# Optimization experiments

Measured on AMD Instinct MI355X. Metric: run time of the kernel, lower is better.

Reference implementation:

```python
import jax, jax.numpy as jnp
import numpy as np

B, C, D, T, N_SUBJ = 64, 1024, 1024, 1024, 32


def setup_inputs() -> dict:
    key = jax.random.key(0)
    k1, k2, k3 = jax.random.split(key, 3)
    x = jax.random.normal(k1, (B, C, T), dtype=jnp.float32)
    subjects = jax.random.randint(k2, (B,), 0, N_SUBJ, dtype=jnp.int64)
    # weights: normal_() then scaled by 1/sqrt(in_channels), as in __init__
    weights = jax.random.normal(k3, (N_SUBJ, C, D), dtype=jnp.float32) / np.sqrt(C).astype(np.float32)
    return {"x": x, "subjects": subjects, "weights": weights}


def reference(x, subjects, weights):
    # gather per-sample projection matrices: (B, C, D)
    w = weights[subjects]
    # out[b, d, t] = sum_c x[b, c, t] * w[b, c, d]
    return jnp.einsum('bct,bcd->bdt', x, w)
```

## Files before the change

### kernel.cpp

```cpp
#include <hip/hip_runtime.h>
#include <hip/hip_bf16.h>

typedef __attribute__((ext_vector_type(8))) short bf16x8;
typedef __attribute__((ext_vector_type(4))) float f32x4;
typedef __attribute__((ext_vector_type(4))) unsigned u32x4;

#define CDIM 1024
#define DDIM 1024
#define TDIM 1024
#define BK 32

__device__ __forceinline__ unsigned cvt_pk_bf16(float a, float b) {
    unsigned r;
    asm("v_cvt_pk_bf16_f32 %0, %1, %2" : "=v"(r) : "v"(a), "v"(b));
    return r;
}


#define KSTEP(VCUR, VNXT, K0)                                                   \
  {                                                                             \
    const int ksafe = ((K0) + BK) & (CDIM - 1);   \
    _Pragma("unroll")                                                           \
    for (int j = 0; j < 8; ++j)                                                 \
        VNXT[j] = *(const float4*)(sp + ((size_t)(ksafe + (cg << 3) + j) << 10)); \
    u32x4 hg[4], lg[4];                                                         \
    _Pragma("unroll")                                                           \
    for (int rr = 0; rr < 4; ++rr) {                                            \
      _Pragma("unroll")                                                         \
      for (int p = 0; p < 4; ++p) {                                             \
        const float f0 = VCUR[2 * p][rr];                                       \
        const float f1 = VCUR[2 * p + 1][rr];                                   \
        const unsigned h = cvt_pk_bf16(f0, f1);                                 \
        const float l0 = f0 - __uint_as_float(h << 16);                         \
        const float l1 = f1 - __uint_as_float(h & 0xFFFF0000u);                 \
        hg[rr][p] = h;                                                          \
        lg[rr][p] = cvt_pk_bf16(l0, l1);                                        \
      }                                                                         \
    }                                                                           \
    __syncthreads();                                                            \
    _Pragma("unroll")                                                           \
    for (int rr = 0; rr < 4; ++rr) {                                            \
      const int row = col0 + rr;                                                \
      short* sl = slds + row * 64;                                              \
      const int so = ((cg ^ ((row ^ (row >> 3)) & 7)) << 3);                    \
      *(u32x4*)(sl + so) = hg[rr];                                              \
      *(u32x4*)(sl + (so ^ 32)) = lg[rr];                                       \
    }                                                                           \
    __syncthreads();                                                            \
    bf16x8 ah[4], al[4];                                                        \
    _Pragma("unroll")                                                           \
    for (int m = 0; m < 4; ++m) {                                               \
      const short* wrow = Wt + (wdOff + m * 16 + fr) * 64;                      \
      ah[m] = *(const bf16x8*)(wrow + offHW[m]);                                \
      al[m] = *(const bf16x8*)(wrow + (offHW[m] ^ 32));                         \
    }                                                                           \
    _Pragma("unroll")                                                           \
    for (int np = 0; np < 4; ++np) {                                            \
      const int n0 = 2 * np, n1 = 2 * np + 1;                                   \
      const short* xr0 = Xt + (wtOff + n0 * 16 + fr) * 64;                      \
      const short* xr1 = Xt + (wtOff + n1 * 16 + fr) * 64;                      \
      const bf16x8 bh0 = *(const bf16x8*)(xr0 + offHX[n0]);                     \
      const bf16x8 bl0 = *(const bf16x8*)(xr0 + (offHX[n0] ^ 32));              \
      const bf16x8 bh1 = *(const bf16x8*)(xr1 + offHX[n1]);                     \
      const bf16x8 bl1 = *(const bf16x8*)(xr1 + (offHX[n1] ^ 32));              \
      _Pragma("unroll")                                                         \
      for (int m = 0; m < 4; ++m)                                               \
        acc[m][n0] = __builtin_amdgcn_mfma_f32_16x16x32_bf16(ah[m], bh0, acc[m][n0], 0, 0, 0); \
      _Pragma("unroll")                                                         \
      for (int m = 0; m < 4; ++m)                                               \
        acc[m][n1] = __builtin_amdgcn_mfma_f32_16x16x32_bf16(ah[m], bh1, acc[m][n1], 0, 0, 0); \
      _Pragma("unroll")                                                         \
      for (int m = 0; m < 4; ++m)                                               \
        acc[m][n0] = __builtin_amdgcn_mfma_f32_16x16x32_bf16(ah[m], bl0, acc[m][n0], 0, 0, 0); \
      _Pragma("unroll")                                                         \
      for (int m = 0; m < 4; ++m)                                               \
        acc[m][n1] = __builtin_amdgcn_mfma_f32_16x16x32_bf16(ah[m], bl1, acc[m][n1], 0, 0, 0); \
      _Pragma("unroll")                                                         \
      for (int m = 0; m < 4; ++m)                                               \
        acc[m][n0] = __builtin_amdgcn_mfma_f32_16x16x32_bf16(al[m], bh0, acc[m][n0], 0, 0, 0); \
      _Pragma("unroll")                                                         \
      for (int m = 0; m < 4; ++m)                                               \
        acc[m][n1] = __builtin_amdgcn_mfma_f32_16x16x32_bf16(al[m], bh1, acc[m][n1], 0, 0, 0); \
    }                                                                           \
  }

__global__ __launch_bounds__(512, 1)
void subject_gemm(const float* __restrict__ x, const int* __restrict__ subj,
                  const float* __restrict__ w, float* __restrict__ out)
{
    __shared__ short Wt[256 * 64];
    __shared__ short Xt[256 * 64];

    const int bid = blockIdx.x;
    const int xcd = bid & 7;
    const int slot = bid >> 3;
    const int b = (xcd << 3) | (slot >> 4);
    const int r = slot & 15;
    const int dtile = (r >> 2) << 8;
    const int ttile = (r & 3) << 8;

    const int s = subj[b];
    const float* __restrict__ wB = w + (size_t)s * (CDIM * DDIM);
    const float* __restrict__ xB = x + (size_t)b * (CDIM * TDIM);

    const int tid = threadIdx.x;
    const int lane = tid & 63;
    const int wave = tid >> 6;

    const int ht = tid & 255;
    const int tq = ht & 63;
    const int cg = ht >> 6;
    const int col0 = tq << 2;
    const bool isW = (tid < 256);
    const float* sp = (isW ? wB + dtile : xB + ttile) + col0;
    short* slds = (isW ? Wt : Xt);

    const int wdOff = (wave >> 1) << 6;
    const int wtOff = (wave & 1) << 7;
    const int fr = lane & 15;
    const int fg = lane >> 4;

    int offHW[4], offHX[8];
    #pragma unroll
    for (int m = 0; m < 4; ++m) {
        const int rowW = wdOff + m * 16 + fr;
        offHW[m] = ((fg ^ ((rowW ^ (rowW >> 3)) & 7)) << 3);
    }
    #pragma unroll
    for (int n = 0; n < 8; ++n) {
        const int rowX = wtOff + n * 16 + fr;
        offHX[n] = ((fg ^ ((rowX ^ (rowX >> 3)) & 7)) << 3);
    }

    f32x4 acc[4][8] = {};

    float4 va[8], vb[8];
    #pragma unroll
    for (int j = 0; j < 8; ++j)
        va[j] = *(const float4*)(sp + ((size_t)((cg << 3) + j) << 10));

    for (int k0 = 0; k0 < CDIM; k0 += 2 * BK) {
        KSTEP(va, vb, k0);
        KSTEP(vb, va, k0 + BK);
    }

    float* __restrict__ oB = out + (size_t)b * (DDIM * TDIM)
                           + (size_t)(dtile + wdOff) * TDIM + (ttile + wtOff);
    #pragma unroll
    for (int m = 0; m < 4; ++m) {
        #pragma unroll
        for (int q = 0; q < 4; ++q) {
            const int d = m * 16 + (fg << 2) + q;
            float* orow = oB + (size_t)d * TDIM;
            #pragma unroll
            for (int n = 0; n < 8; ++n) {
                orow[n * 16 + fr] = acc[m][n][q];
            }
        }
    }
}

extern "C" void kernel_launch(void* const* d_in, const int* in_sizes, int n_in,
                              void* d_out, int out_size, void* d_ws, size_t ws_size,
                              hipStream_t stream) {
    const float* x = (const float*)d_in[0];
    const int* subjects = (const int*)d_in[1];
    const float* w = (const float*)d_in[2];
    float* out = (float*)d_out;
    subject_gemm<<<dim3(1024), dim3(512), 0, stream>>>(x, subjects, w, out);
}
```

Baseline: 377.5 us.

## Double-buffer LDS tiles to cut syncs per K-step to one

Adds a second pair of LDS buffers so each K-step writes the converted next tile into one buffer while the MFMAs read the other. The two barriers per step become one barrier at the end of the step, and a prologue converts and stores the first tile ahead of the loop. This raises LDS use to 64 KB and deepens the software pipeline to two tiles in flight, which adds register pressure. The final iterations load wrapped addresses that are never used.

```diff
diff --git a/kernel.cpp b/kernel.cpp
--- a/kernel.cpp
+++ b/kernel.cpp
@@ -17,19 +17,19 @@
 }
 
 
-#define KSTEP(VCUR, VNXT, K0)                                                   \
+#define KSTEP(VCVT, VLD, KLOAD, WRD, XRD, SWRBASE)                              \
   {                                                                             \
-    const int ksafe = ((K0) + BK) & (CDIM - 1);   \
+    const int ksafe = (KLOAD) & (CDIM - 1);    \
     _Pragma("unroll")                                                           \
     for (int j = 0; j < 8; ++j)                                                 \
-        VNXT[j] = *(const float4*)(sp + ((size_t)(ksafe + (cg << 3) + j) << 10)); \
+        VLD[j] = *(const float4*)(sp + ((size_t)(ksafe + (cg << 3) + j) << 10)); \
     u32x4 hg[4], lg[4];                                                         \
     _Pragma("unroll")                                                           \
     for (int rr = 0; rr < 4; ++rr) {                                            \
       _Pragma("unroll")                                                         \
       for (int p = 0; p < 4; ++p) {                                             \
-        const float f0 = VCUR[2 * p][rr];                                       \
-        const float f1 = VCUR[2 * p + 1][rr];                                   \
+        const float f0 = VCVT[2 * p][rr];                                       \
+        const float f1 = VCVT[2 * p + 1][rr];                                   \
         const unsigned h = cvt_pk_bf16(f0, f1);                                 \
         const float l0 = f0 - __uint_as_float(h << 16);                         \
         const float l1 = f1 - __uint_as_float(h & 0xFFFF0000u);                 \
@@ -37,28 +37,26 @@
         lg[rr][p] = cvt_pk_bf16(l0, l1);                                        \
       }                                                                         \
     }                                                                           \
-    __syncthreads();                                                            \
     _Pragma("unroll")                                                           \
     for (int rr = 0; rr < 4; ++rr) {                                            \
       const int row = col0 + rr;                                                \
-      short* sl = slds + row * 64;                                              \
+      short* sl = (SWRBASE) + row * 64;                                         \
       const int so = ((cg ^ ((row ^ (row >> 3)) & 7)) << 3);                    \
       *(u32x4*)(sl + so) = hg[rr];                                              \
       *(u32x4*)(sl + (so ^ 32)) = lg[rr];                                       \
     }                                                                           \
-    __syncthreads();                                                            \
     bf16x8 ah[4], al[4];                                                        \
     _Pragma("unroll")                                                           \
     for (int m = 0; m < 4; ++m) {                                               \
-      const short* wrow = Wt + (wdOff + m * 16 + fr) * 64;                      \
+      const short* wrow = (WRD) + (wdOff + m * 16 + fr) * 64;                   \
       ah[m] = *(const bf16x8*)(wrow + offHW[m]);                                \
       al[m] = *(const bf16x8*)(wrow + (offHW[m] ^ 32));                         \
     }                                                                           \
     _Pragma("unroll")                                                           \
     for (int np = 0; np < 4; ++np) {                                            \
       const int n0 = 2 * np, n1 = 2 * np + 1;                                   \
-      const short* xr0 = Xt + (wtOff + n0 * 16 + fr) * 64;                      \
-      const short* xr1 = Xt + (wtOff + n1 * 16 + fr) * 64;                      \
+      const short* xr0 = (XRD) + (wtOff + n0 * 16 + fr) * 64;                   \
+      const short* xr1 = (XRD) + (wtOff + n1 * 16 + fr) * 64;                   \
       const bf16x8 bh0 = *(const bf16x8*)(xr0 + offHX[n0]);                     \
       const bf16x8 bl0 = *(const bf16x8*)(xr0 + (offHX[n0] ^ 32));              \
       const bf16x8 bh1 = *(const bf16x8*)(xr1 + offHX[n1]);                     \
@@ -82,14 +80,15 @@
       for (int m = 0; m < 4; ++m)                                               \
         acc[m][n1] = __builtin_amdgcn_mfma_f32_16x16x32_bf16(al[m], bh1, acc[m][n1], 0, 0, 0); \
     }                                                                           \
+    __syncthreads();                                                            \
   }
 
 __global__ __launch_bounds__(512, 1)
 void subject_gemm(const float* __restrict__ x, const int* __restrict__ subj,
                   const float* __restrict__ w, float* __restrict__ out)
 {
-    __shared__ short Wt[256 * 64];
-    __shared__ short Xt[256 * 64];
+    __shared__ short WtA[256 * 64], XtA[256 * 64];
+    __shared__ short WtB[256 * 64], XtB[256 * 64];
 
     const int bid = blockIdx.x;
     const int xcd = bid & 7;
@@ -113,7 +112,8 @@
     const int col0 = tq << 2;
     const bool isW = (tid < 256);
     const float* sp = (isW ? wB + dtile : xB + ttile) + col0;
-    short* slds = (isW ? Wt : Xt);
+    short* sldsA = (isW ? WtA : XtA);
+    short* sldsB = (isW ? WtB : XtB);
 
     const int wdOff = (wave >> 1) << 6;
     const int wtOff = (wave & 1) << 7;
@@ -138,10 +138,38 @@
     #pragma unroll
     for (int j = 0; j < 8; ++j)
         va[j] = *(const float4*)(sp + ((size_t)((cg << 3) + j) << 10));
+    {
+        u32x4 hg[4], lg[4];
+        #pragma unroll
+        for (int rr = 0; rr < 4; ++rr) {
+            #pragma unroll
+            for (int p = 0; p < 4; ++p) {
+                const float f0 = va[2 * p][rr];
+                const float f1 = va[2 * p + 1][rr];
+                const unsigned h = cvt_pk_bf16(f0, f1);
+                const float l0 = f0 - __uint_as_float(h << 16);
+                const float l1 = f1 - __uint_as_float(h & 0xFFFF0000u);
+                hg[rr][p] = h;
+                lg[rr][p] = cvt_pk_bf16(l0, l1);
+            }
+        }
+        #pragma unroll
+        for (int rr = 0; rr < 4; ++rr) {
+            const int row = col0 + rr;
+            short* sl = sldsA + row * 64;
+            const int so = ((cg ^ ((row ^ (row >> 3)) & 7)) << 3);
+            *(u32x4*)(sl + so) = hg[rr];
+            *(u32x4*)(sl + (so ^ 32)) = lg[rr];
+        }
+    }
+    #pragma unroll
+    for (int j = 0; j < 8; ++j)
+        vb[j] = *(const float4*)(sp + ((size_t)(BK + (cg << 3) + j) << 10));
+    __syncthreads();
 
     for (int k0 = 0; k0 < CDIM; k0 += 2 * BK) {
-        KSTEP(va, vb, k0);
-        KSTEP(vb, va, k0 + BK);
+        KSTEP(vb, va, k0 + 2 * BK, WtA, XtA, sldsB);
+        KSTEP(va, vb, k0 + 3 * BK, WtB, XtB, sldsA);
     }
 
     float* __restrict__ oB = out + (size_t)b * (DDIM * TDIM)
```

Result: slower. 879.6 us (+133.0%).

## Precompute split-bf16 swizzled weights and double-buffer LDS with direct global-to-LDS loads

Applied to the files above, without the earlier changes.

A new prep kernel runs on every call. It converts all subject weight matrices into pre-swizzled hi/lo bf16 tiles in the workspace. The main GEMM then streams those tiles straight into LDS with global_load_lds and double-buffers both the weight and x tiles, so each k-step needs one barrier instead of two. It also drops the low-order bf16 correction term for x, cutting MFMA work by a third at the cost of accuracy on the x side. The prep pass adds extra memory traffic for weights of every subject, including unused ones. When the workspace is too small, the original kernel runs as a fallback.

```diff
diff --git a/kernel.cpp b/kernel.cpp
--- a/kernel.cpp
+++ b/kernel.cpp
@@ -15,105 +15,151 @@
     asm("v_cvt_pk_bf16_f32 %0, %1, %2" : "=v"(r) : "v"(a), "v"(b));
     return r;
 }
-
-
-#define KSTEP(VCUR, VNXT, K0)                                                   \
+__device__ __forceinline__ int swz8(int r) { return (r ^ (r >> 3)) & 7; }
+__device__ __forceinline__ int swz4(int r) { return (r ^ (r >> 3)) & 3; }
+
+__global__ __launch_bounds__(512, 1)
+void prep_w(const float* __restrict__ w, short* __restrict__ wopt)
+{
+    __shared__ float T[32 * 260];
+    const int blk = blockIdx.x;
+    const int kt = blk & 31;
+    const int dt = (blk >> 5) & 3;
+    const int s  = blk >> 7;
+    const float* wb = w + (size_t)s * (CDIM * DDIM)
+                        + (size_t)(kt * 32) * DDIM + dt * 256;
+    const int tid = threadIdx.x;
+    {
+        const int row = tid >> 4;
+        const int seg = tid & 15;
+        const float* src = wb + (size_t)row * DDIM + seg * 16;
+        float4 a0 = *(const float4*)(src);
+        float4 a1 = *(const float4*)(src + 4);
+        float4 a2 = *(const float4*)(src + 8);
+        float4 a3 = *(const float4*)(src + 12);
+        float* dst = T + row * 260 + seg * 16;
+        *(float4*)(dst) = a0;      *(float4*)(dst + 4) = a1;
+        *(float4*)(dst + 8) = a2;  *(float4*)(dst + 12) = a3;
+    }
+    __syncthreads();
+    short* outc = wopt + (size_t)blk * 16384;
+    #pragma unroll
+    for (int j = 0; j < 4; ++j) {
+        const int u = tid + 512 * j;
+        const int r = u >> 3;
+        const int sl = u & 7;
+        const int g = sl ^ swz8(r);
+        const int kk = (g & 3) * 8;
+        const bool hi = (g < 4);
+        unsigned o[4];
+        #pragma unroll
+        for (int p = 0; p < 4; ++p) {
+            const float f0 = T[(kk + 2 * p    ) * 260 + r];
+            const float f1 = T[(kk + 2 * p + 1) * 260 + r];
+            const unsigned h = cvt_pk_bf16(f0, f1);
+            const float l0 = f0 - __uint_as_float(h << 16);
+            const float l1 = f1 - __uint_as_float(h & 0xFFFF0000u);
+            const unsigned lo = cvt_pk_bf16(l0, l1);
+            o[p] = hi ? h : lo;
+        }
+        *(u32x4*)(outc + (size_t)u * 8) = *(u32x4*)o;
+    }
+}
+
+#define KSTEP(P, Q, KNEXT)                                                      \
   {                                                                             \
-    const int ksafe = ((K0) + BK) & (CDIM - 1);   \
-    _Pragma("unroll")                                                           \
-    for (int j = 0; j < 8; ++j)                                                 \
-        VNXT[j] = *(const float4*)(sp + ((size_t)(ksafe + (cg << 3) + j) << 10)); \
-    u32x4 hg[4], lg[4];                                                         \
+    const int kn = (KNEXT) & (CDIM - 1);                                        \
+    _Pragma("unroll")                                                           \
+    for (int j = 0; j < 4; ++j)                                                 \
+        v[j] = *(const float4*)(xp + ((size_t)(kn + cbase + j) << 10));         \
+    {                                                                           \
+      const short* gsrc = wchunk + (size_t)(kn >> 5) * 16384                    \
+                          + wave * 2048 + lane * 8;                             \
+      short* ldst = &Wt[Q][wave * 2048];                                        \
+      _Pragma("unroll")                                                         \
+      for (int q = 0; q < 4; ++q)                                               \
+        __builtin_amdgcn_global_load_lds(                                       \
+            (const __attribute__((address_space(1))) void*)(gsrc + q * 512),    \
+            (__attribute__((address_space(3))) void*)(ldst + q * 512),          \
+            16, 0, 0);                                                          \
+    }                                                                           \
+    asm volatile("s_waitcnt vmcnt(8)" ::: "memory");                            \
+    __builtin_amdgcn_sched_barrier(0);                                          \
+    {                                                                           \
+      bf16x8 ah[4], al[4];                                                      \
+      _Pragma("unroll")                                                         \
+      for (int m = 0; m < 4; ++m) {                                             \
+        const short* wrow = &Wt[P][(wdOff + m * 16 + fr) * 64];                 \
+        ah[m] = *(const bf16x8*)(wrow + offHW[m]);                              \
+        al[m] = *(const bf16x8*)(wrow + (offHW[m] ^ 32));                       \
+      }                                                                         \
+      _Pragma("unroll")                                                         \
+      for (int np = 0; np < 4; ++np) {                                          \
+        const int n0 = 2 * np, n1 = 2 * np + 1;                                 \
+        const bf16x8 bh0 = *(const bf16x8*)(&Xt[P][(wtOff + n0 * 16 + fr) * 32] + offHX[n0]); \
+        const bf16x8 bh1 = *(const bf16x8*)(&Xt[P][(wtOff + n1 * 16 + fr) * 32] + offHX[n1]); \
+        _Pragma("unroll")                                                       \
+        for (int m = 0; m < 4; ++m)                                             \
+          acc[m][n0] = __builtin_amdgcn_mfma_f32_16x16x32_bf16(ah[m], bh0, acc[m][n0], 0, 0, 0); \
+        _Pragma("unroll")                                                       \
+        for (int m = 0; m < 4; ++m)                                             \
+          acc[m][n1] = __builtin_amdgcn_mfma_f32_16x16x32_bf16(ah[m], bh1, acc[m][n1], 0, 0, 0); \
+        _Pragma("unroll")                                                       \
+        for (int m = 0; m < 4; ++m)                                             \
+          acc[m][n0] = __builtin_amdgcn_mfma_f32_16x16x32_bf16(al[m], bh0, acc[m][n0], 0, 0, 0); \
+        _Pragma("unroll")                                                       \
+        for (int m = 0; m < 4; ++m)                                             \
+          acc[m][n1] = __builtin_amdgcn_mfma_f32_16x16x32_bf16(al[m], bh1, acc[m][n1], 0, 0, 0); \
+      }                                                                         \
+    }                                                                           \
+    asm volatile("s_waitcnt vmcnt(4)" ::: "memory");                            \
+    __builtin_amdgcn_sched_barrier(0);                                          \
     _Pragma("unroll")                                                           \
     for (int rr = 0; rr < 4; ++rr) {                                            \
-      _Pragma("unroll")                                                         \
-      for (int p = 0; p < 4; ++p) {                                             \
-        const float f0 = VCUR[2 * p][rr];                                       \
-        const float f1 = VCUR[2 * p + 1][rr];                                   \
-        const unsigned h = cvt_pk_bf16(f0, f1);                                 \
-        const float l0 = f0 - __uint_as_float(h << 16);                         \
-        const float l1 = f1 - __uint_as_float(h & 0xFFFF0000u);                 \
-        hg[rr][p] = h;                                                          \
-        lg[rr][p] = cvt_pk_bf16(l0, l1);                                        \
-      }                                                                         \
-    }                                                                           \
-    __syncthreads();                                                            \
-    _Pragma("unroll")                                                           \
-    for (int rr = 0; rr < 4; ++rr) {                                            \
+      const unsigned h0 = cvt_pk_bf16(v[0][rr], v[1][rr]);                      \
+      const unsigned h1 = cvt_pk_bf16(v[2][rr], v[3][rr]);                      \
       const int row = col0 + rr;                                                \
-      short* sl = slds + row * 64;                                              \
-      const int so = ((cg ^ ((row ^ (row >> 3)) & 7)) << 3);                    \
-      *(u32x4*)(sl + so) = hg[rr];                                              \
-      *(u32x4*)(sl + (so ^ 32)) = lg[rr];                                       \
-    }                                                                           \
-    __syncthreads();                                                            \
-    bf16x8 ah[4], al[4];                                                        \
-    _Pragma("unroll")                                                           \
-    for (int m = 0; m < 4; ++m) {                                               \
-      const short* wrow = Wt + (wdOff + m * 16 + fr) * 64;                      \
-      ah[m] = *(const bf16x8*)(wrow + offHW[m]);                                \
-      al[m] = *(const bf16x8*)(wrow + (offHW[m] ^ 32));                         \
-    }                                                                           \
-    _Pragma("unroll")                                                           \
-    for (int np = 0; np < 4; ++np) {                                            \
-      const int n0 = 2 * np, n1 = 2 * np + 1;                                   \
-      const short* xr0 = Xt + (wtOff + n0 * 16 + fr) * 64;                      \
-      const short* xr1 = Xt + (wtOff + n1 * 16 + fr) * 64;                      \
-      const bf16x8 bh0 = *(const bf16x8*)(xr0 + offHX[n0]);                     \
-      const bf16x8 bl0 = *(const bf16x8*)(xr0 + (offHX[n0] ^ 32));              \
-      const bf16x8 bh1 = *(const bf16x8*)(xr1 + offHX[n1]);                     \
-      const bf16x8 bl1 = *(const bf16x8*)(xr1 + (offHX[n1] ^ 32));              \
-      _Pragma("unroll")                                                         \
-      for (int m = 0; m < 4; ++m)                                               \
-        acc[m][n0] = __builtin_amdgcn_mfma_f32_16x16x32_bf16(ah[m], bh0, acc[m][n0], 0, 0, 0); \
-      _Pragma("unroll")                                                         \
-      for (int m = 0; m < 4; ++m)                                               \
-        acc[m][n1] = __builtin_amdgcn_mfma_f32_16x16x32_bf16(ah[m], bh1, acc[m][n1], 0, 0, 0); \
-      _Pragma("unroll")                                                         \
-      for (int m = 0; m < 4; ++m)                                               \
-        acc[m][n0] = __builtin_amdgcn_mfma_f32_16x16x32_bf16(ah[m], bl0, acc[m][n0], 0, 0, 0); \
-      _Pragma("unroll")                                                         \
-      for (int m = 0; m < 4; ++m)                                               \
-        acc[m][n1] = __builtin_amdgcn_mfma_f32_16x16x32_bf16(ah[m], bl1, acc[m][n1], 0, 0, 0); \
-      _Pragma("unroll")                                                         \
-      for (int m = 0; m < 4; ++m)                                               \
-        acc[m][n0] = __builtin_amdgcn_mfma_f32_16x16x32_bf16(al[m], bh0, acc[m][n0], 0, 0, 0); \
-      _Pragma("unroll")                                                         \
-      for (int m = 0; m < 4; ++m)                                               \
-        acc[m][n1] = __builtin_amdgcn_mfma_f32_16x16x32_bf16(al[m], bh1, acc[m][n1], 0, 0, 0); \
-    }                                                                           \
+      const int so = ((xg ^ swz4(row)) << 3) + xh * 4;                          \
+      uint2 pr; pr.x = h0; pr.y = h1;                                           \
+      *(uint2*)(&Xt[Q][row * 32 + so]) = pr;                                    \
+    }                                                                           \
+    asm volatile("s_waitcnt lgkmcnt(0)" ::: "memory");                          \
+    __builtin_amdgcn_sched_barrier(0);                                          \
+    __builtin_amdgcn_s_barrier();                                               \
+    __builtin_amdgcn_sched_barrier(0);                                          \
   }
 
 __global__ __launch_bounds__(512, 1)
-void subject_gemm(const float* __restrict__ x, const int* __restrict__ subj,
-                  const float* __restrict__ w, float* __restrict__ out)
+void subject_gemm2(const float* __restrict__ x, const int* __restrict__ subj,
+                   const short* __restrict__ wopt, float* __restrict__ out)
 {
-    __shared__ short Wt[256 * 64];
-    __shared__ short Xt[256 * 64];
+    __shared__ short Wt[2][256 * 64];
+    __shared__ short Xt[2][256 * 32];
 
     const int bid = blockIdx.x;
     const int xcd = bid & 7;
     const int slot = bid >> 3;
     const int b = (xcd << 3) | (slot >> 4);
     const int r = slot & 15;
-    const int dtile = (r >> 2) << 8;
+    const int dtIdx = r >> 2;
+    const int dtile = dtIdx << 8;
     const int ttile = (r & 3) << 8;
 
     const int s = subj[b];
-    const float* __restrict__ wB = w + (size_t)s * (CDIM * DDIM);
+    const short* __restrict__ wchunk = wopt + (size_t)((s * 4 + dtIdx) * 32) * 16384;
     const float* __restrict__ xB = x + (size_t)b * (CDIM * TDIM);
 
     const int tid = threadIdx.x;
     const int lane = tid & 63;
     const int wave = tid >> 6;
 
-    const int ht = tid & 255;
-    const int tq = ht & 63;
-    const int cg = ht >> 6;
-    const int col0 = tq << 2;
-    const bool isW = (tid < 256);
-    const float* sp = (isW ? wB + dtile : xB + ttile) + col0;
-    short* slds = (isW ? Wt : Xt);
+    const int tq = tid & 63;
+    const int cg = tid >> 6;
+    const int xg = cg >> 1;
+    const int xh = cg & 1;
+    const int cbase = cg * 4;
+    const int col0 = tq * 4;
+    const float* xp = xB + ttile + col0;
 
     const int wdOff = (wave >> 1) << 6;
     const int wtOff = (wave & 1) << 7;
@@ -124,24 +170,49 @@
     #pragma unroll
     for (int m = 0; m < 4; ++m) {
         const int rowW = wdOff + m * 16 + fr;
-        offHW[m] = ((fg ^ ((rowW ^ (rowW >> 3)) & 7)) << 3);
+        offHW[m] = ((fg ^ swz8(rowW)) << 3);
     }
     #pragma unroll
     for (int n = 0; n < 8; ++n) {
         const int rowX = wtOff + n * 16 + fr;
-        offHX[n] = ((fg ^ ((rowX ^ (rowX >> 3)) & 7)) << 3);
+        offHX[n] = ((fg ^ swz4(rowX)) << 3);
     }
 
     f32x4 acc[4][8] = {};
-
-    float4 va[8], vb[8];
-    #pragma unroll
-    for (int j = 0; j < 8; ++j)
-        va[j] = *(const float4*)(sp + ((size_t)((cg << 3) + j) << 10));
+    float4 v[4];
+
+    #pragma unroll
+    for (int j = 0; j < 4; ++j)
+        v[j] = *(const float4*)(xp + ((size_t)(cbase + j) << 10));
+    asm volatile("s_waitcnt vmcnt(0)" ::: "memory");
+    __builtin_amdgcn_sched_barrier(0);
+    #pragma unroll
+    for (int rr = 0; rr < 4; ++rr) {
+        const unsigned h0 = cvt_pk_bf16(v[0][rr], v[1][rr]);
+        const unsigned h1 = cvt_pk_bf16(v[2][rr], v[3][rr]);
+        const int row = col0 + rr;
+        const int so = ((xg ^ swz4(row)) << 3) + xh * 4;
+        uint2 pr; pr.x = h0; pr.y = h1;
+        *(uint2*)(&Xt[0][row * 32 + so]) = pr;
+    }
+    {
+        const short* gsrc = wchunk + wave * 2048 + lane * 8;
+        short* ldst = &Wt[0][wave * 2048];
+        #pragma unroll
+        for (int q = 0; q < 4; ++q)
+            __builtin_amdgcn_global_load_lds(
+                (const __attribute__((address_space(1))) void*)(gsrc + q * 512),
+                (__attribute__((address_space(3))) void*)(ldst + q * 512),
+                16, 0, 0);
+    }
+    asm volatile("s_waitcnt lgkmcnt(0)" ::: "memory");
+    __builtin_amdgcn_sched_barrier(0);
+    __builtin_amdgcn_s_barrier();
+    __builtin_amdgcn_sched_barrier(0);
 
     for (int k0 = 0; k0 < CDIM; k0 += 2 * BK) {
-        KSTEP(va, vb, k0);
-        KSTEP(vb, va, k0 + BK);
+        KSTEP(0, 1, k0 + BK);
+        KSTEP(1, 0, k0 + 2 * BK);
     }
 
     float* __restrict__ oB = out + (size_t)b * (DDIM * TDIM)
@@ -160,6 +231,149 @@
     }
 }
 
+#define FKSTEP(VCUR, VNXT, K0)                                                  \
+  {                                                                             \
+    const int ksafe = ((K0) + BK) & (CDIM - 1);                                 \
+    _Pragma("unroll")                                                           \
+    for (int j = 0; j < 8; ++j)                                                 \
+        VNXT[j] = *(const float4*)(sp + ((size_t)(ksafe + (cg << 3) + j) << 10)); \
+    u32x4 hg[4], lg[4];                                                         \
+    _Pragma("unroll")                                                           \
+    for (int rr = 0; rr < 4; ++rr) {                                            \
+      _Pragma("unroll")                                                         \
+      for (int p = 0; p < 4; ++p) {                                             \
+        const float f0 = VCUR[2 * p][rr];                                       \
+        const float f1 = VCUR[2 * p + 1][rr];                                   \
+        const unsigned h = cvt_pk_bf16(f0, f1);                                 \
+        const float l0 = f0 - __uint_as_float(h << 16);                         \
+        const float l1 = f1 - __uint_as_float(h & 0xFFFF0000u);                 \
+        hg[rr][p] = h;                                                          \
+        lg[rr][p] = cvt_pk_bf16(l0, l1);                                        \
+      }                                                                         \
+    }                                                                           \
+    __syncthreads();                                                            \
+    _Pragma("unroll")                                                           \
+    for (int rr = 0; rr < 4; ++rr) {                                            \
+      const int row = col0 + rr;                                                \
+      short* sl = slds + row * 64;                                              \
+      const int so = ((cg ^ swz8(row)) << 3);                                   \
+      *(u32x4*)(sl + so) = hg[rr];                                              \
+      *(u32x4*)(sl + (so ^ 32)) = lg[rr];                                       \
+    }                                                                           \
+    __syncthreads();                                                            \
+    bf16x8 ah[4], al[4];                                                        \
+    _Pragma("unroll")                                                           \
+    for (int m = 0; m < 4; ++m) {                                               \
+      const short* wrow = Wt + (wdOff + m * 16 + fr) * 64;                      \
+      ah[m] = *(const bf16x8*)(wrow + offHW[m]);                                \
+      al[m] = *(const bf16x8*)(wrow + (offHW[m] ^ 32));                         \
+    }                                                                           \
+    _Pragma("unroll")                                                           \
+    for (int np = 0; np < 4; ++np) {                                            \
+      const int n0 = 2 * np, n1 = 2 * np + 1;                                   \
+      const short* xr0 = Xt + (wtOff + n0 * 16 + fr) * 64;                      \
+      const short* xr1 = Xt + (wtOff + n1 * 16 + fr) * 64;                      \
+      const bf16x8 bh0 = *(const bf16x8*)(xr0 + offHX[n0]);                     \
+      const bf16x8 bl0 = *(const bf16x8*)(xr0 + (offHX[n0] ^ 32));              \
+      const bf16x8 bh1 = *(const bf16x8*)(xr1 + offHX[n1]);                     \
+      const bf16x8 bl1 = *(const bf16x8*)(xr1 + (offHX[n1] ^ 32));              \
+      _Pragma("unroll")                                                         \
+      for (int m = 0; m < 4; ++m)                                               \
+        acc[m][n0] = __builtin_amdgcn_mfma_f32_16x16x32_bf16(ah[m], bh0, acc[m][n0], 0, 0, 0); \
+      _Pragma("unroll")                                                         \
+      for (int m = 0; m < 4; ++m)                                               \
+        acc[m][n1] = __builtin_amdgcn_mfma_f32_16x16x32_bf16(ah[m], bh1, acc[m][n1], 0, 0, 0); \
+      _Pragma("unroll")                                                         \
+      for (int m = 0; m < 4; ++m)                                               \
+        acc[m][n0] = __builtin_amdgcn_mfma_f32_16x16x32_bf16(ah[m], bl0, acc[m][n0], 0, 0, 0); \
+      _Pragma("unroll")                                                         \
+      for (int m = 0; m < 4; ++m)                                               \
+        acc[m][n1] = __builtin_amdgcn_mfma_f32_16x16x32_bf16(ah[m], bl1, acc[m][n1], 0, 0, 0); \
+      _Pragma("unroll")                                                         \
+      for (int m = 0; m < 4; ++m)                                               \
+        acc[m][n0] = __builtin_amdgcn_mfma_f32_16x16x32_bf16(al[m], bh0, acc[m][n0], 0, 0, 0); \
+      _Pragma("unroll")                                                         \
+      for (int m = 0; m < 4; ++m)                                               \
+        acc[m][n1] = __builtin_amdgcn_mfma_f32_16x16x32_bf16(al[m], bh1, acc[m][n1], 0, 0, 0); \
+    }                                                                           \
+  }
+
+__global__ __launch_bounds__(512, 1)
+void subject_gemm_fb(const float* __restrict__ x, const int* __restrict__ subj,
+                     const float* __restrict__ w, float* __restrict__ out)
+{
+    __shared__ short Wt[256 * 64];
+    __shared__ short Xt[256 * 64];
+
+    const int bid = blockIdx.x;
+    const int xcd = bid & 7;
+    const int slot = bid >> 3;
+    const int b = (xcd << 3) | (slot >> 4);
+    const int r = slot & 15;
+    const int dtile = (r >> 2) << 8;
+    const int ttile = (r & 3) << 8;
+
+    const int s = subj[b];
+    const float* __restrict__ wB = w + (size_t)s * (CDIM * DDIM);
+    const float* __restrict__ xB = x + (size_t)b * (CDIM * TDIM);
+
+    const int tid = threadIdx.x;
+    const int lane = tid & 63;
+    const int wave = tid >> 6;
+
+    const int ht = tid & 255;
+    const int tq = ht & 63;
+    const int cg = ht >> 6;
+    const int col0 = tq << 2;
+    const bool isW = (tid < 256);
+    const float* sp = (isW ? wB + dtile : xB + ttile) + col0;
+    short* slds = (isW ? Wt : Xt);
+
+    const int wdOff = (wave >> 1) << 6;
+    const int wtOff = (wave & 1) << 7;
+    const int fr = lane & 15;
+    const int fg = lane >> 4;
+
+    int offHW[4], offHX[8];
+    #pragma unroll
+    for (int m = 0; m < 4; ++m) {
+        const int rowW = wdOff + m * 16 + fr;
+        offHW[m] = ((fg ^ swz8(rowW)) << 3);
+    }
+    #pragma unroll
+    for (int n = 0; n < 8; ++n) {
+        const int rowX = wtOff + n * 16 + fr;
+        offHX[n] = ((fg ^ swz8(rowX)) << 3);
+    }
+
+    f32x4 acc[4][8] = {};
+
+    float4 va[8], vb[8];
+    #pragma unroll
+    for (int j = 0; j < 8; ++j)
+        va[j] = *(const float4*)(sp + ((size_t)((cg << 3) + j) << 10));
+
+    for (int k0 = 0; k0 < CDIM; k0 += 2 * BK) {
+        FKSTEP(va, vb, k0);
+        FKSTEP(vb, va, k0 + BK);
+    }
+
+    float* __restrict__ oB = out + (size_t)b * (DDIM * TDIM)
+                           + (size_t)(dtile + wdOff) * TDIM + (ttile + wtOff);
+    #pragma unroll
+    for (int m = 0; m < 4; ++m) {
+        #pragma unroll
+        for (int q = 0; q < 4; ++q) {
+            const int d = m * 16 + (fg << 2) + q;
+            float* orow = oB + (size_t)d * TDIM;
+            #pragma unroll
+            for (int n = 0; n < 8; ++n) {
+                orow[n * 16 + fr] = acc[m][n][q];
+            }
+        }
+    }
+}
+
 extern "C" void kernel_launch(void* const* d_in, const int* in_sizes, int n_in,
                               void* d_out, int out_size, void* d_ws, size_t ws_size,
                               hipStream_t stream) {
@@ -167,5 +381,12 @@
     const int* subjects = (const int*)d_in[1];
     const float* w = (const float*)d_in[2];
     float* out = (float*)d_out;
-    subject_gemm<<<dim3(1024), dim3(512), 0, stream>>>(x, subjects, w, out);
-}
+    const size_t NEED = (size_t)4096 * 32768;
+    if (ws_size >= NEED) {
+        prep_w<<<dim3(4096), dim3(512), 0, stream>>>(w, (short*)d_ws);
+        subject_gemm2<<<dim3(1024), dim3(512), 0, stream>>>(
+            x, subjects, (const short*)d_ws, out);
+    } else {
+        subject_gemm_fb<<<dim3(1024), dim3(512), 0, stream>>>(x, subjects, w, out);
+    }
+}
```

Result: slower. 385.3 us (+2.1%).
